# Kernel optimization log

Measured on AMD Instinct MI355X. Metric: run time of the kernel, lower is better.

Reference implementation:

```python
import jax, jax.numpy as jnp
import numpy as np

B, S, HID, NH = 2, 2048, 1024, 16
HD = HID // NH  # 64


def setup_inputs() -> dict:
    key = jax.random.key(0)
    ks = jax.random.split(key, 10)
    sc = 0.02
    return {
        "hidden_states": jax.random.normal(ks[0], (B, S, HID), jnp.float32),
        "attention_mask": jnp.zeros((B, 1, 1, S), jnp.float32),
        "struct_attn_mask": jax.random.normal(ks[1], (B, S, S), jnp.float32),
        "Wq": jax.random.normal(ks[2], (HID, HID), jnp.float32) * sc,
        "bq": jnp.zeros((HID,), jnp.float32),
        "Wk": jax.random.normal(ks[3], (HID, HID), jnp.float32) * sc,
        "bk": jnp.zeros((HID,), jnp.float32),
        "Wv": jax.random.normal(ks[4], (HID, HID), jnp.float32) * sc,
        "bv": jnp.zeros((HID,), jnp.float32),
        "struct_gate": jnp.full((NH,), 0.1, jnp.float32),
    }


def _heads(x):
    # [B,S,HID] -> [B,NH,S,HD]
    return x.reshape(B, S, NH, HD).transpose(0, 2, 1, 3)


def reference(hidden_states, attention_mask, struct_attn_mask, Wq, bq, Wk, bk, Wv, bv, struct_gate):
    q = _heads(hidden_states @ Wq.T + bq)
    k = _heads(hidden_states @ Wk.T + bk)
    v = _heads(hidden_states @ Wv.T + bv)
    scores = jnp.einsum("bhqd,bhkd->bhqk", q, k) / np.sqrt(HD).astype(np.float32)
    scores = scores + attention_mask
    scores = scores + struct_attn_mask[:, None, :, :] * struct_gate[None, :, None, None]
    probs = jax.nn.softmax(scores, axis=-1)  # dropout p=0 (eval) -> no-op
    ctx = jnp.einsum("bhqk,bhkd->bhqd", probs, v)
    ctx = ctx.transpose(0, 2, 1, 3).reshape(B, S, HID)
    return (ctx,)
```

## Files before the change

kernel.cpp:

```cpp
#include <hip/hip_runtime.h>
#include <hip/hip_bf16.h>
#include <cmath>

#define S_LEN 2048
#define HIDN  1024
#define NHEAD 16
#define HDIM  64
#define NBAT  2

static constexpr long NA = (long)NBAT * S_LEN * HIDN;
static constexpr long NW = (long)HIDN * HIDN;
static constexpr long NM = (long)NBAT * S_LEN * S_LEN;
static constexpr long NAM = (long)NBAT * S_LEN;

typedef __attribute__((ext_vector_type(8))) __bf16 bf16x8;
typedef __attribute__((ext_vector_type(4))) float f32x4;
typedef __attribute__((ext_vector_type(16))) float f32x16;
typedef __attribute__((ext_vector_type(4))) unsigned short u16x4;

#define LOG2E 1.44269504088896340736f

__device__ __forceinline__ unsigned short f2bf(float f) {
  __hip_bfloat16 h = __float2bfloat16(f);
  unsigned short u;
  __builtin_memcpy(&u, &h, 2);
  return u;
}

__device__ __forceinline__ float bfu2f(unsigned short u) {
  unsigned v = (unsigned)u << 16;
  float f;
  __builtin_memcpy(&f, &v, 4);
  return f;
}

__device__ __forceinline__ unsigned cvtpk(float a, float b) {
  unsigned r;
  asm volatile("v_cvt_pk_bf16_f32 %0, %1, %2" : "=v"(r) : "v"(a), "v"(b));
  return r;
}

__device__ __forceinline__ void gload_lds16(const void* g, void* l) {
  __builtin_amdgcn_global_load_lds(
      (const __attribute__((address_space(1))) void*)g,
      (__attribute__((address_space(3))) void*)l, 16, 0, 0);
}

__global__ __launch_bounds__(256) void convert_kernel(
    const float* __restrict__ hs, const float* __restrict__ wq,
    const float* __restrict__ wk, const float* __restrict__ wv,
    const float* __restrict__ mask, const float* __restrict__ amask,
    __hip_bfloat16* __restrict__ Abf, __hip_bfloat16* __restrict__ Wcat,
    __hip_bfloat16* __restrict__ Mbf, float* __restrict__ amg) {
  const long tot4 = (NA + 3 * NW + NM + NAM) >> 2;
  for (long i4 = (long)blockIdx.x * blockDim.x + threadIdx.x; i4 < tot4;
       i4 += (long)gridDim.x * blockDim.x) {
    long i = i4 << 2;
    if (i < NA + 3 * NW + NM) {
      const float* s;
      __hip_bfloat16* dq;
      if (i < NA)               { s = hs + i;                   dq = Abf + i; }
      else if (i < NA + NW)     { s = wq + (i - NA);            dq = Wcat + (i - NA); }
      else if (i < NA + 2 * NW) { s = wk + (i - NA - NW);       dq = Wcat + (i - NA); }
      else if (i < NA + 3 * NW) { s = wv + (i - NA - 2 * NW);   dq = Wcat + (i - NA); }
      else                      { s = mask + (i - NA - 3 * NW); dq = Mbf + (i - NA - 3 * NW); }
      float4 v = *(const float4*)s;
      union { unsigned short u[4]; uint2 p; } o;
      o.u[0] = f2bf(v.x); o.u[1] = f2bf(v.y); o.u[2] = f2bf(v.z); o.u[3] = f2bf(v.w);
      *(uint2*)dq = o.p;
    } else {
      long j = i - (NA + 3 * NW + NM);
      float4 v = *(const float4*)(amask + j);
      v.x *= LOG2E; v.y *= LOG2E; v.z *= LOG2E; v.w *= LOG2E;
      *(float4*)(amg + j) = v;
    }
  }
}

__global__ __launch_bounds__(256) void qkv_gemm(
    const __hip_bfloat16* __restrict__ A, const __hip_bfloat16* __restrict__ Bw,
    const float* __restrict__ bq, const float* __restrict__ bk,
    const float* __restrict__ bv, __hip_bfloat16* __restrict__ qb,
    __hip_bfloat16* __restrict__ kb, __hip_bfloat16* __restrict__ vb) {
  __shared__ __hip_bfloat16 sA[128 * 32];
  __shared__ __hip_bfloat16 sB[128 * 32];

  int bid = blockIdx.x;
  int cpx = gridDim.x >> 3;
  int wg = (bid & 7) * cpx + (bid >> 3);
  int bm = wg / 24, bn = wg % 24;
  int tid = threadIdx.x, lane = tid & 63, wid = tid >> 6;
  int wr = wid >> 1, wc = wid & 1;
  int lr = lane & 15, hi = lane >> 4;
  int srow = lane >> 2, scol = (lane & 3) * 8;

  f32x4 acc[4][4] = {};

  for (int kt = 0; kt < 32; ++kt) {
    int k0 = kt * 32;
#pragma unroll
    for (int cc = 0; cc < 2; ++cc) {
      int c = wid * 2 + cc;
      const __hip_bfloat16* ga =
          A + ((size_t)(bm * 128 + c * 16 + srow) * 1024 + k0 + scol);
      gload_lds16(ga, (char*)sA + c * 1024);
      const __hip_bfloat16* gb =
          Bw + ((size_t)(bn * 128 + c * 16 + srow) * 1024 + k0 + scol);
      gload_lds16(gb, (char*)sB + c * 1024);
    }
    __syncthreads();
    bf16x8 af[4], bf[4];
#pragma unroll
    for (int mt = 0; mt < 4; ++mt)
      af[mt] = *(const bf16x8*)((const char*)sA +
                                ((wr * 64 + mt * 16 + lr) * 32 + hi * 8) * 2);
#pragma unroll
    for (int nt = 0; nt < 4; ++nt)
      bf[nt] = *(const bf16x8*)((const char*)sB +
                                ((wc * 64 + nt * 16 + lr) * 32 + hi * 8) * 2);
#pragma unroll
    for (int mt = 0; mt < 4; ++mt)
#pragma unroll
      for (int nt = 0; nt < 4; ++nt)
        acc[mt][nt] =
            __builtin_amdgcn_mfma_f32_16x16x32_bf16(af[mt], bf[nt], acc[mt][nt], 0, 0, 0);
    __syncthreads();
  }

  const float c2 = LOG2E / 8.0f;
#pragma unroll
  for (int nt = 0; nt < 4; ++nt) {
    int nb = bn * 128 + wc * 64 + nt * 16;
    int t = nb >> 10;
    int rem = nb & 1023;
    const float* bp = (t == 0) ? bq : (t == 1) ? bk : bv;
    __hip_bfloat16* ob = (t == 0) ? qb : (t == 1) ? kb : vb;
    float scl = (t == 0) ? c2 : 1.0f;
    int h = rem >> 6, d0 = rem & 63;
    float bias = bp[rem + lr];
    int d = d0 + lr;
#pragma unroll
    for (int mt = 0; mt < 4; ++mt) {
#pragma unroll
      for (int r = 0; r < 4; ++r) {
        int m = bm * 128 + wr * 64 + mt * 16 + hi * 4 + r;
        int b = m >> 11, s = m & 2047;
        size_t off = (((size_t)(b * NHEAD + h)) * S_LEN + s) * HDIM + d;
        ob[off] = __float2bfloat16((acc[mt][nt][r] + bias) * scl);
      }
    }
  }
}

__global__ __launch_bounds__(256) void vtrans_kernel(
    const __hip_bfloat16* __restrict__ vb, __hip_bfloat16* __restrict__ vt) {
  __shared__ __hip_bfloat16 tile[64][72];
  int bh = blockIdx.x >> 5;
  int st = blockIdx.x & 31;
  int t = threadIdx.x;
  int r8 = t >> 3, c8 = (t & 7) * 8;
#pragma unroll
  for (int p = 0; p < 2; ++p) {
    int row = p * 32 + r8;
    bf16x8 v = *(const bf16x8*)(vb + ((size_t)bh * S_LEN + st * 64 + row) * HDIM + c8);
    *(bf16x8*)&tile[row][c8] = v;
  }
  __syncthreads();
#pragma unroll
  for (int p = 0; p < 2; ++p) {
    int d = p * 32 + r8;
    union { unsigned short u[8]; bf16x8 v; } o;
#pragma unroll
    for (int j = 0; j < 8; ++j) {
      __hip_bfloat16 e = tile[c8 + j][d];
      __builtin_memcpy(&o.u[j], &e, 2);
    }
    *(bf16x8*)(vt + ((size_t)bh * HDIM + d) * S_LEN + st * 64 + c8) = o.v;
  }
}

__global__ __launch_bounds__(512, 4) void attn_kernel(
    const __hip_bfloat16* __restrict__ qb, const __hip_bfloat16* __restrict__ kbuf,
    const __hip_bfloat16* __restrict__ vt, const __hip_bfloat16* __restrict__ Mbf,
    const float* __restrict__ amg, const float* __restrict__ gate,
    float* __restrict__ out) {
  __shared__ alignas(16) char smem[73728];
  __shared__ float mlb[4][2][32];

  int bid = blockIdx.x;
  int wg = (bid & 7) * 64 + (bid >> 3);
  int bi = wg >> 8;
  int h = (wg >> 4) & 15;
  int qt = wg & 15;
  int bh = bi * NHEAD + h;

  int tid = threadIdx.x;
  int lane = tid & 63, wid = tid >> 6;
  int grp = wid >> 2, w4 = wid & 3;
  int l31 = lane & 31, hi2 = lane >> 5;
  int qbase = qt * 128 + w4 * 32;
  int qrow = qbase + l31;
  int kbase = grp << 10;
  float g2 = gate[h] * LOG2E;

  const char* Kb = (const char*)kbuf + (size_t)bh * S_LEN * 128;
  const char* Vb = (const char*)vt + (size_t)bh * HDIM * S_LEN * 2;
  const char* Mrow = (const char*)Mbf + ((size_t)bi * S_LEN + qrow) * S_LEN * 2 + hi2 * 8;

  bf16x8 qf[4];
  {
    const __hip_bfloat16* qp = qb + ((size_t)bh * S_LEN + qrow) * HDIM + hi2 * 8;
#pragma unroll
    for (int dc = 0; dc < 4; ++dc) qf[dc] = *(const bf16x8*)(qp + dc * 16);
  }

  int r8 = lane >> 3, ch = lane & 7;
  float* amL = (float*)(smem + 65536 + grp * 4096);

  auto stage = [&](int buf, int t) {
    int k0 = kbase + t * 64;
    char* kdst = smem + buf * 32768 + grp * 16384 + w4 * 2048;
    char* vdst = kdst + 8192;
#pragma unroll
    for (int c = 0; c < 2; ++c) {
      int row = w4 * 16 + c * 8 + r8;
      gload_lds16(Kb + (size_t)(k0 + row) * 128 + ((ch ^ r8) << 4), kdst + c * 1024);
      gload_lds16(Vb + (size_t)row * 4096 + (size_t)k0 * 2 + ((ch ^ r8) << 4),
                  vdst + c * 1024);
    }
  };

  u16x4 mn0[4], mn1[4];
#pragma unroll
  for (int rp = 0; rp < 4; ++rp) {
    mn0[rp] = *(const u16x4*)(Mrow + (size_t)(kbase + rp * 8) * 2);
    mn1[rp] = *(const u16x4*)(Mrow + (size_t)(kbase + 32 + rp * 8) * 2);
  }

  stage(0, 0);
  gload_lds16((const char*)amg + ((size_t)bi * S_LEN + kbase + w4 * 256) * 4,
              (char*)amL + w4 * 1024);
  __syncthreads();

  f32x16 O = {}, O2 = {};
  float m = -INFINITY, l = 0.f;

  for (int t = 0; t < 16; ++t) {
    int cur = t & 1;
    if (t < 15) stage(cur ^ 1, t + 1);
    const char* sK = smem + cur * 32768 + grp * 16384;
    const char* sV = sK + 8192;

#pragma unroll
    for (int ss = 0; ss < 2; ++ss) {
      int klocal = t * 64 + ss * 32;

      f32x16 st = {};
#pragma unroll
      for (int dc = 0; dc < 4; ++dc) {
        int row = ss * 32 + l31;
        bf16x8 kf = *(const bf16x8*)(sK + row * 128 +
                                     (((dc * 2 + hi2) ^ (l31 & 7)) << 4));
        st = __builtin_amdgcn_mfma_f32_32x32x16_bf16(kf, qf[dc], st, 0, 0, 0);
      }

      float pmax = -3.4e38f;
#pragma unroll
      for (int rp = 0; rp < 4; ++rp) {
        float4 am = *(const float4*)(amL + klocal + rp * 8 + hi2 * 4);
        union { u16x4 v; unsigned short e[4]; } mv;
        mv.v = ss ? mn1[rp] : mn0[rp];
        float s0 = fmaf(bfu2f(mv.e[0]), g2, st[rp * 4 + 0] + am.x);
        float s1 = fmaf(bfu2f(mv.e[1]), g2, st[rp * 4 + 1] + am.y);
        float s2 = fmaf(bfu2f(mv.e[2]), g2, st[rp * 4 + 2] + am.z);
        float s3 = fmaf(bfu2f(mv.e[3]), g2, st[rp * 4 + 3] + am.w);
        st[rp * 4 + 0] = s0; st[rp * 4 + 1] = s1;
        st[rp * 4 + 2] = s2; st[rp * 4 + 3] = s3;
        pmax = fmaxf(pmax, fmaxf(fmaxf(s0, s1), fmaxf(s2, s3)));
      }

      if (t < 15) {
        int kn = kbase + (t + 1) * 64 + ss * 32;
#pragma unroll
        for (int rp = 0; rp < 4; ++rp) {
          u16x4 nv = *(const u16x4*)(Mrow + (size_t)(kn + rp * 8) * 2);
          if (ss) mn1[rp] = nv; else mn0[rp] = nv;
        }
      }

      pmax = fmaxf(pmax, __shfl_xor(pmax, 32));
      if (__any(pmax > m + 8.f)) {
        float mnew = fmaxf(m, pmax);
        float alpha = exp2f(m - mnew);
        m = mnew;
        l *= alpha;
        O *= alpha;
        O2 *= alpha;
      }

      float rs0 = 0.f, rs1 = 0.f, rs2 = 0.f, rs3 = 0.f;
#pragma unroll
      for (int rp = 0; rp < 4; ++rp) {
        float p0 = exp2f(st[rp * 4 + 0] - m);
        float p1 = exp2f(st[rp * 4 + 1] - m);
        float p2 = exp2f(st[rp * 4 + 2] - m);
        float p3 = exp2f(st[rp * 4 + 3] - m);
        st[rp * 4 + 0] = p0; st[rp * 4 + 1] = p1;
        st[rp * 4 + 2] = p2; st[rp * 4 + 3] = p3;
        rs0 += p0; rs1 += p1; rs2 += p2; rs3 += p3;
      }
      float rs = (rs0 + rs1) + (rs2 + rs3);
      rs += __shfl_xor(rs, 32);
      l += rs;

#pragma unroll
      for (int ks = 0; ks < 2; ++ks) {
        int rp = ks * 2;
        unsigned A0 = cvtpk(st[rp * 4 + 0], st[rp * 4 + 1]);
        unsigned A1 = cvtpk(st[rp * 4 + 2], st[rp * 4 + 3]);
        unsigned B0 = cvtpk(st[rp * 4 + 4], st[rp * 4 + 5]);
        unsigned B1 = cvtpk(st[rp * 4 + 6], st[rp * 4 + 7]);
        asm volatile("v_permlane32_swap_b32 %0, %1" : "+v"(A0), "+v"(B0));
        asm volatile("v_permlane32_swap_b32 %0, %1" : "+v"(A1), "+v"(B1));
        union { unsigned w[4]; bf16x8 v; } Bf;
        Bf.w[0] = A0; Bf.w[1] = A1; Bf.w[2] = B0; Bf.w[3] = B1;
        int vc = ss * 4 + ks * 2 + hi2;
        bf16x8 v0 = *(const bf16x8*)(sV + l31 * 128 + ((vc ^ (l31 & 7)) << 4));
        bf16x8 v1 = *(const bf16x8*)(sV + (32 + l31) * 128 + ((vc ^ (l31 & 7)) << 4));
        O = __builtin_amdgcn_mfma_f32_32x32x16_bf16(v0, Bf.v, O, 0, 0, 0);
        O2 = __builtin_amdgcn_mfma_f32_32x32x16_bf16(v1, Bf.v, O2, 0, 0, 0);
      }
    }
    __syncthreads();
  }

  float* mbuf = (float*)smem + w4 * (32 * 68);
  if (grp == 1) {
    if (hi2 == 0) { mlb[w4][0][l31] = m; mlb[w4][1][l31] = l; }
#pragma unroll
    for (int dt = 0; dt < 2; ++dt)
#pragma unroll
      for (int rq = 0; rq < 4; ++rq) {
        int d0 = dt * 32 + 8 * rq + 4 * hi2;
        const f32x16& Ox = dt ? O2 : O;
        f32x4 v = {Ox[rq * 4 + 0], Ox[rq * 4 + 1], Ox[rq * 4 + 2], Ox[rq * 4 + 3]};
        *(f32x4*)(mbuf + l31 * 68 + d0) = v;
      }
  }
  __syncthreads();
  if (grp == 0) {
    float m1 = mlb[w4][0][l31], l1 = mlb[w4][1][l31];
    float mx = fmaxf(m, m1);
    float a0 = exp2f(m - mx), a1 = exp2f(m1 - mx);
    float linv = 1.0f / (a0 * l + a1 * l1);
    a0 *= linv; a1 *= linv;
    float* orow = out + ((size_t)bi * S_LEN + qrow) * HIDN + h * HDIM;
#pragma unroll
    for (int dt = 0; dt < 2; ++dt)
#pragma unroll
      for (int rq = 0; rq < 4; ++rq) {
        int d0 = dt * 32 + 8 * rq + 4 * hi2;
        const f32x16& Ox = dt ? O2 : O;
        f32x4 v1 = *(const f32x4*)(mbuf + l31 * 68 + d0);
        float4 o;
        o.x = Ox[rq * 4 + 0] * a0 + v1[0] * a1;
        o.y = Ox[rq * 4 + 1] * a0 + v1[1] * a1;
        o.z = Ox[rq * 4 + 2] * a0 + v1[2] * a1;
        o.w = Ox[rq * 4 + 3] * a0 + v1[3] * a1;
        *(float4*)(orow + d0) = o;
      }
  }
}

extern "C" void kernel_launch(void* const* d_in, const int* in_sizes, int n_in,
                              void* d_out, int out_size, void* d_ws, size_t ws_size,
                              hipStream_t stream) {
  const float* hs    = (const float*)d_in[0];
  const float* amask = (const float*)d_in[1];
  const float* smask = (const float*)d_in[2];
  const float* Wq    = (const float*)d_in[3];
  const float* bq    = (const float*)d_in[4];
  const float* Wk    = (const float*)d_in[5];
  const float* bk    = (const float*)d_in[6];
  const float* Wv    = (const float*)d_in[7];
  const float* bv    = (const float*)d_in[8];
  const float* gate  = (const float*)d_in[9];

  char* ws = (char*)d_ws;
  __hip_bfloat16* Abf  = (__hip_bfloat16*)(ws);
  __hip_bfloat16* Wcat = (__hip_bfloat16*)(ws + 8388608);
  __hip_bfloat16* qb   = (__hip_bfloat16*)(ws + 8388608 + 6291456);
  __hip_bfloat16* kb   = qb + NA;
  __hip_bfloat16* vb   = kb + NA;
  __hip_bfloat16* Mbf  = vb + NA;
  float*          amg  = (float*)(Mbf + NM);
  __hip_bfloat16* vt   = Abf;

  convert_kernel<<<2048, 256, 0, stream>>>(hs, Wq, Wk, Wv, smask, amask, Abf, Wcat, Mbf, amg);
  qkv_gemm<<<768, 256, 0, stream>>>(Abf, Wcat, bq, bk, bv, qb, kb, vb);
  vtrans_kernel<<<1024, 256, 0, stream>>>(vb, vt);
  attn_kernel<<<512, 512, 0, stream>>>(qb, kb, vt, Mbf, amg, gate, (float*)d_out);
}
```

Measured before the change: 144.6 us.

## Write V transposed directly from QKV GEMM epilogue and preload mask into score accumulator

```diff
diff --git a/kernel.cpp b/kernel.cpp
--- a/kernel.cpp
+++ b/kernel.cpp
@@ -81,7 +81,7 @@
     const __hip_bfloat16* __restrict__ A, const __hip_bfloat16* __restrict__ Bw,
     const float* __restrict__ bq, const float* __restrict__ bk,
     const float* __restrict__ bv, __hip_bfloat16* __restrict__ qb,
-    __hip_bfloat16* __restrict__ kb, __hip_bfloat16* __restrict__ vb) {
+    __hip_bfloat16* __restrict__ kb, __hip_bfloat16* __restrict__ vtb) {
   __shared__ __hip_bfloat16 sA[128 * 32];
   __shared__ __hip_bfloat16 sB[128 * 32];
 
@@ -134,48 +134,28 @@
     int t = nb >> 10;
     int rem = nb & 1023;
     const float* bp = (t == 0) ? bq : (t == 1) ? bk : bv;
-    __hip_bfloat16* ob = (t == 0) ? qb : (t == 1) ? kb : vb;
     float scl = (t == 0) ? c2 : 1.0f;
-    int h = rem >> 6, d0 = rem & 63;
+    int h = rem >> 6, d0r = rem & 63;
     float bias = bp[rem + lr];
-    int d = d0 + lr;
+    int d = d0r + lr;
 #pragma unroll
     for (int mt = 0; mt < 4; ++mt) {
-#pragma unroll
-      for (int r = 0; r < 4; ++r) {
-        int m = bm * 128 + wr * 64 + mt * 16 + hi * 4 + r;
-        int b = m >> 11, s = m & 2047;
-        size_t off = (((size_t)(b * NHEAD + h)) * S_LEN + s) * HDIM + d;
-        ob[off] = __float2bfloat16((acc[mt][nt][r] + bias) * scl);
-      }
-    }
-  }
-}
-
-__global__ __launch_bounds__(256) void vtrans_kernel(
-    const __hip_bfloat16* __restrict__ vb, __hip_bfloat16* __restrict__ vt) {
-  __shared__ __hip_bfloat16 tile[64][72];
-  int bh = blockIdx.x >> 5;
-  int st = blockIdx.x & 31;
-  int t = threadIdx.x;
-  int r8 = t >> 3, c8 = (t & 7) * 8;
-#pragma unroll
-  for (int p = 0; p < 2; ++p) {
-    int row = p * 32 + r8;
-    bf16x8 v = *(const bf16x8*)(vb + ((size_t)bh * S_LEN + st * 64 + row) * HDIM + c8);
-    *(bf16x8*)&tile[row][c8] = v;
-  }
-  __syncthreads();
-#pragma unroll
-  for (int p = 0; p < 2; ++p) {
-    int d = p * 32 + r8;
-    union { unsigned short u[8]; bf16x8 v; } o;
-#pragma unroll
-    for (int j = 0; j < 8; ++j) {
-      __hip_bfloat16 e = tile[c8 + j][d];
-      __builtin_memcpy(&o.u[j], &e, 2);
-    }
-    *(bf16x8*)(vt + ((size_t)bh * HDIM + d) * S_LEN + st * 64 + c8) = o.v;
+      int m0 = bm * 128 + wr * 64 + mt * 16 + hi * 4;
+      int b = m0 >> 11, s = m0 & 2047;
+      if (t == 2) {
+        union { unsigned short u[4]; uint2 p; } o;
+#pragma unroll
+        for (int r = 0; r < 4; ++r) o.u[r] = f2bf(acc[mt][nt][r] + bias);
+        *(uint2*)(vtb + (((size_t)(b * NHEAD + h) * HDIM + d) * S_LEN + s)) = o.p;
+      } else {
+        __hip_bfloat16* ob = (t == 0) ? qb : kb;
+#pragma unroll
+        for (int r = 0; r < 4; ++r) {
+          size_t off = (((size_t)(b * NHEAD + h)) * S_LEN + (s + r)) * HDIM + d;
+          ob[off] = __float2bfloat16((acc[mt][nt][r] + bias) * scl);
+        }
+      }
+    }
   }
 }
 
@@ -255,7 +235,27 @@
     for (int ss = 0; ss < 2; ++ss) {
       int klocal = t * 64 + ss * 32;
 
-      f32x16 st = {};
+      f32x16 st;
+#pragma unroll
+      for (int rp = 0; rp < 4; ++rp) {
+        float4 am = *(const float4*)(amL + klocal + rp * 8 + hi2 * 4);
+        union { u16x4 v; unsigned short e[4]; } mv;
+        mv.v = ss ? mn1[rp] : mn0[rp];
+        st[rp * 4 + 0] = fmaf(bfu2f(mv.e[0]), g2, am.x);
+        st[rp * 4 + 1] = fmaf(bfu2f(mv.e[1]), g2, am.y);
+        st[rp * 4 + 2] = fmaf(bfu2f(mv.e[2]), g2, am.z);
+        st[rp * 4 + 3] = fmaf(bfu2f(mv.e[3]), g2, am.w);
+      }
+
+      if (t < 15) {
+        int kn = kbase + (t + 1) * 64 + ss * 32;
+#pragma unroll
+        for (int rp = 0; rp < 4; ++rp) {
+          u16x4 nv = *(const u16x4*)(Mrow + (size_t)(kn + rp * 8) * 2);
+          if (ss) mn1[rp] = nv; else mn0[rp] = nv;
+        }
+      }
+
 #pragma unroll
       for (int dc = 0; dc < 4; ++dc) {
         int row = ss * 32 + l31;
@@ -266,28 +266,9 @@
 
       float pmax = -3.4e38f;
 #pragma unroll
-      for (int rp = 0; rp < 4; ++rp) {
-        float4 am = *(const float4*)(amL + klocal + rp * 8 + hi2 * 4);
-        union { u16x4 v; unsigned short e[4]; } mv;
-        mv.v = ss ? mn1[rp] : mn0[rp];
-        float s0 = fmaf(bfu2f(mv.e[0]), g2, st[rp * 4 + 0] + am.x);
-        float s1 = fmaf(bfu2f(mv.e[1]), g2, st[rp * 4 + 1] + am.y);
-        float s2 = fmaf(bfu2f(mv.e[2]), g2, st[rp * 4 + 2] + am.z);
-        float s3 = fmaf(bfu2f(mv.e[3]), g2, st[rp * 4 + 3] + am.w);
-        st[rp * 4 + 0] = s0; st[rp * 4 + 1] = s1;
-        st[rp * 4 + 2] = s2; st[rp * 4 + 3] = s3;
-        pmax = fmaxf(pmax, fmaxf(fmaxf(s0, s1), fmaxf(s2, s3)));
-      }
-
-      if (t < 15) {
-        int kn = kbase + (t + 1) * 64 + ss * 32;
-#pragma unroll
-        for (int rp = 0; rp < 4; ++rp) {
-          u16x4 nv = *(const u16x4*)(Mrow + (size_t)(kn + rp * 8) * 2);
-          if (ss) mn1[rp] = nv; else mn0[rp] = nv;
-        }
-      }
-
+      for (int rp = 0; rp < 4; ++rp)
+        pmax = fmaxf(pmax, fmaxf(fmaxf(st[rp * 4 + 0], st[rp * 4 + 1]),
+                                 fmaxf(st[rp * 4 + 2], st[rp * 4 + 3])));
       pmax = fmaxf(pmax, __shfl_xor(pmax, 32));
       if (__any(pmax > m + 8.f)) {
         float mnew = fmaxf(m, pmax);
@@ -391,13 +372,11 @@
   __hip_bfloat16* Wcat = (__hip_bfloat16*)(ws + 8388608);
   __hip_bfloat16* qb   = (__hip_bfloat16*)(ws + 8388608 + 6291456);
   __hip_bfloat16* kb   = qb + NA;
-  __hip_bfloat16* vb   = kb + NA;
-  __hip_bfloat16* Mbf  = vb + NA;
+  __hip_bfloat16* vtr  = kb + NA;
+  __hip_bfloat16* Mbf  = vtr + NA;
   float*          amg  = (float*)(Mbf + NM);
-  __hip_bfloat16* vt   = Abf;
 
   convert_kernel<<<2048, 256, 0, stream>>>(hs, Wq, Wk, Wv, smask, amask, Abf, Wcat, Mbf, amg);
-  qkv_gemm<<<768, 256, 0, stream>>>(Abf, Wcat, bq, bk, bv, qb, kb, vb);
-  vtrans_kernel<<<1024, 256, 0, stream>>>(vb, vt);
-  attn_kernel<<<512, 512, 0, stream>>>(qb, kb, vt, Mbf, amg, gate, (float*)d_out);
-}
+  qkv_gemm<<<768, 256, 0, stream>>>(Abf, Wcat, bq, bk, bv, qb, kb, vtr);
+  attn_kernel<<<512, 512, 0, stream>>>(qb, kb, vtr, Mbf, amg, gate, (float*)d_out);
+}
```

Result: faster. 137.2 us (-5.1%).
